# Optimization experiments

Measured on AMD Instinct MI355X. Metric: run time of the kernel, lower is better.

## Reference

```python
import jax, jax.numpy as jnp
import numpy as np

IMG_W, IMG_H = 960.0, 512.0          # NETWORK.IMAGE_SIZE
HM_W, HM_H = 240.0, 128.0            # NETWORK.HEATMAP_SIZE (w, h)
GRID_SIZE = (8000.0, 8000.0, 2000.0)
CUBE = (80, 80, 20)
SPACE_CENTER = (0.0, -500.0, 800.0)


def _make_grid():
    # compute_grid: meshgrid(indexing='ij'), flattened to [nbins, 3]
    gx = np.linspace(-GRID_SIZE[0] / 2, GRID_SIZE[0] / 2, CUBE[0]) + SPACE_CENTER[0]
    gy = np.linspace(-GRID_SIZE[1] / 2, GRID_SIZE[1] / 2, CUBE[1]) + SPACE_CENTER[1]
    gz = np.linspace(-GRID_SIZE[2] / 2, GRID_SIZE[2] / 2, CUBE[2]) + SPACE_CENTER[2]
    X, Y, Z = np.meshgrid(gx, gy, gz, indexing='ij')
    return jnp.asarray(np.stack([X.ravel(), Y.ravel(), Z.ravel()], 1), jnp.float32)


def setup_inputs() -> dict:
    key = jax.random.key(0)
    ks = jax.random.split(key, 8)
    n, B, J, H, W = 5, 4, 15, 128, 240
    heatmaps = jax.random.uniform(ks[0], (n, B, J, H, W), jnp.float32)
    # cameras: rotate about z per view, positioned so all grid points have depth > 0
    thetas = np.linspace(0.0, 2 * np.pi, n, endpoint=False)
    Rs = np.zeros((n, B, 3, 3), np.float32)
    for v, th in enumerate(thetas):
        c, s = np.cos(th), np.sin(th)
        Rs[v, :] = np.array([[c, -s, 0.0], [s, c, 0.0], [0.0, 0.0, 1.0]], np.float32)
    cam_R = jnp.asarray(Rs)
    cam_T = jnp.asarray(np.tile(np.array([0.0, 0.0, -5000.0], np.float32), (n, B, 1))) \
        + 50.0 * jax.random.normal(ks[1], (n, B, 3), jnp.float32)
    cam_f = 1500.0 + 20.0 * jax.random.normal(ks[2], (n, B, 2), jnp.float32)
    cam_c = jnp.asarray([IMG_W / 2, IMG_H / 2], jnp.float32) \
        + 5.0 * jax.random.normal(ks[3], (n, B, 2), jnp.float32)
    cam_k = jnp.asarray(np.tile(np.array([-0.01, 0.001, 0.0], np.float32), (n, B, 1))) \
        + 1e-4 * jax.random.normal(ks[4], (n, B, 3), jnp.float32)
    cam_p = 1e-3 * jax.random.normal(ks[5], (n, B, 2), jnp.float32)
    center = jnp.asarray([IMG_W / 2, IMG_H / 2], jnp.float32) \
        + 10.0 * jax.random.normal(ks[6], (n, B, 2), jnp.float32)
    scale = jnp.asarray([IMG_W / 200.0, IMG_H / 200.0], jnp.float32) \
        * (1.0 + 0.05 * jax.random.uniform(ks[7], (n, B, 2), jnp.float32))
    return {"heatmaps": heatmaps, "cam_R": cam_R, "cam_T": cam_T, "cam_f": cam_f,
            "cam_c": cam_c, "cam_k": cam_k, "cam_p": cam_p, "center": center,
            "scale": scale}


def _forward(heatmaps, cam_R, cam_T, cam_f, cam_c, cam_k, cam_p, center, scale):
    n, B, J, Hd, Wd = heatmaps.shape
    grid = _make_grid()                                   # [N, 3]
    N = grid.shape[0]
    # --- project_pose (pinhole + radial/tangential distortion) ---
    diff = grid[None, None] - cam_T[:, :, None, :]        # [v,b,N,3]
    xcam = jnp.einsum('vbij,vbnj->vbni', cam_R, diff)     # [v,b,N,3]
    y = xcam[..., :2] / (xcam[..., 2:3] + 1e-5)
    r2 = jnp.sum(y * y, -1)                               # [v,b,N]
    radial = 1.0 + cam_k[..., 0:1] * r2 + cam_k[..., 1:2] * r2 ** 2 + cam_k[..., 2:3] * r2 ** 3
    tan = cam_p[..., 0:1] * y[..., 1] + cam_p[..., 1:2] * y[..., 0]
    y = y * (radial + 2.0 * tan)[..., None] \
        + jnp.stack([cam_p[..., 1], cam_p[..., 0]], -1)[:, :, None, :] * r2[..., None]
    pix = cam_f[:, :, None, :] * y + cam_c[:, :, None, :]  # [v,b,N,2]
    # --- bounding: inside image of size (width, height) = 2*center ---
    wh = 2.0 * center                                      # [v,b,2]
    bounding = ((pix[..., 0] >= 0) & (pix[..., 1] >= 0)
                & (pix[..., 0] < wh[..., 0:1]) & (pix[..., 1] < wh[..., 1:2])
                ).astype(heatmaps.dtype)                   # [v,b,N]
    maxwh = jnp.maximum(wh[..., 0], wh[..., 1])[..., None, None]
    pix = jnp.clip(pix, -1.0, maxwh)
    # --- get_transform(center, scale, 0, img_size) + do_transform ---
    hs = 200.0 * scale                                     # [v,b,2]
    img = jnp.asarray([IMG_W, IMG_H], heatmaps.dtype)
    t_scale = img / hs                                     # diag of affine
    t_off = img * (-center / hs + 0.5)
    xy = pix * t_scale[:, :, None, :] + t_off[:, :, None, :]
    # scale to heatmap resolution, then to normalized [-1,1] (align_corners=True)
    xy = xy * (jnp.asarray([HM_W, HM_H], heatmaps.dtype) / img)
    sg = xy / jnp.asarray([HM_W - 1, HM_H - 1], heatmaps.dtype) * 2.0 - 1.0
    sg = jnp.clip(sg, -1.1, 1.1)
    # --- bilinear grid_sample, align_corners=True, zeros padding ---
    px = (sg[..., 0] + 1.0) * 0.5 * (Wd - 1)
    py = (sg[..., 1] + 1.0) * 0.5 * (Hd - 1)
    x0 = jnp.floor(px)
    y0 = jnp.floor(py)
    wx = px - x0
    wy = py - y0
    x0i = x0.astype(jnp.int32)
    y0i = y0.astype(jnp.int32)
    flat = heatmaps.reshape(n, B, J, Hd * Wd)

    def corner(xi, yi):
        valid = ((xi >= 0) & (xi < Wd) & (yi >= 0) & (yi < Hd)).astype(heatmaps.dtype)
        idx = jnp.clip(yi, 0, Hd - 1) * Wd + jnp.clip(xi, 0, Wd - 1)   # [v,b,N]
        g = jnp.take_along_axis(flat, idx[:, :, None, :], axis=3)       # [v,b,J,N]
        return g * valid[:, :, None, :]

    val = (corner(x0i, y0i) * ((1 - wx) * (1 - wy))[:, :, None, :]
           + corner(x0i + 1, y0i) * (wx * (1 - wy))[:, :, None, :]
           + corner(x0i, y0i + 1) * ((1 - wx) * wy)[:, :, None, :]
           + corner(x0i + 1, y0i + 1) * (wx * wy)[:, :, None, :])       # [v,b,J,N]
    # --- per-view cube = bounding * sampled; combine over views ---
    cubes_v = bounding[:, :, None, :] * val
    num = jnp.sum(cubes_v * bounding[:, :, None, :], axis=0)            # [b,J,N]
    den = jnp.sum(bounding, axis=0)[:, None, :] + 1e-6
    cubes = jnp.clip(num / den, 0.0, 1.0).reshape(B, J, CUBE[0], CUBE[1], CUBE[2])
    grids = jnp.broadcast_to(grid, (B, N, 3))
    return cubes, grids


def reference(heatmaps, cam_R, cam_T, cam_f, cam_c, cam_k, cam_p, center, scale):
    return _forward(heatmaps, cam_R, cam_T, cam_f, cam_c, cam_k, cam_p, center, scale)
```

## Files before the change

kernel.cpp:

```cpp
#include <hip/hip_runtime.h>

#define NV 5
#define NB 4
#define NJ 15
#define HD 128
#define WD 240
#define CX 80
#define CY 80
#define CZ 20
#define NPTS (CX*CY*CZ)
#define JP 16

struct ViewSample {
    float w[4];
    int   cx0, cx1, cy0, cy1;
    float bnd;
};

__device__ __forceinline__ ViewSample project_one_view(
    float gx, float gy, float gz,
    const float* __restrict__ cam_R, const float* __restrict__ cam_T,
    const float* __restrict__ cam_f, const float* __restrict__ cam_c,
    const float* __restrict__ cam_k, const float* __restrict__ cam_p,
    const float* __restrict__ center, const float* __restrict__ scale,
    int cb)
{
    const float* R = cam_R + cb*9;
    const float* T = cam_T + cb*3;
    float fx = cam_f[cb*2+0], fy = cam_f[cb*2+1];
    float ccx = cam_c[cb*2+0], ccy = cam_c[cb*2+1];
    float k0 = cam_k[cb*3+0], k1 = cam_k[cb*3+1], k2 = cam_k[cb*3+2];
    float p0 = cam_p[cb*2+0], p1 = cam_p[cb*2+1];
    float cenx = center[cb*2+0], ceny = center[cb*2+1];
    float scx = scale[cb*2+0],  scy = scale[cb*2+1];

    float dx = gx - T[0], dy = gy - T[1], dz = gz - T[2];
    float xc = R[0]*dx + R[1]*dy + R[2]*dz;
    float yc = R[3]*dx + R[4]*dy + R[5]*dz;
    float zc = R[6]*dx + R[7]*dy + R[8]*dz;
    float invz = 1.0f / (zc + 1e-5f);
    float ux = xc * invz, uy = yc * invz;
    float r2 = ux*ux + uy*uy;
    float radial = 1.0f + k0*r2 + k1*(r2*r2) + k2*(r2*r2*r2);
    float tn = p0*uy + p1*ux;
    float m  = radial + 2.0f*tn;
    float xd = ux*m + p1*r2;
    float yd = uy*m + p0*r2;
    float pixx = fx*xd + ccx;
    float pixy = fy*yd + ccy;

    float whx = 2.0f*cenx, why = 2.0f*ceny;
    float bnd = (pixx >= 0.0f && pixy >= 0.0f && pixx < whx && pixy < why) ? 1.0f : 0.0f;
    float mwh = fmaxf(whx, why);
    pixx = fminf(fmaxf(pixx, -1.0f), mwh);
    pixy = fminf(fmaxf(pixy, -1.0f), mwh);

    float hsx = 200.0f*scx, hsy = 200.0f*scy;
    float xyx = (pixx * (960.0f/hsx) + 960.0f*(-cenx/hsx + 0.5f)) * 0.25f;
    float xyy = (pixy * (512.0f/hsy) + 512.0f*(-ceny/hsy + 0.5f)) * 0.25f;
    float sgx = (xyx / 239.0f) * 2.0f - 1.0f;
    float sgy = (xyy / 127.0f) * 2.0f - 1.0f;
    sgx = fminf(fmaxf(sgx, -1.1f), 1.1f);
    sgy = fminf(fmaxf(sgy, -1.1f), 1.1f);

    float pxf = (sgx + 1.0f) * 0.5f * 239.0f;
    float pyf = (sgy + 1.0f) * 0.5f * 127.0f;
    float x0f = floorf(pxf), y0f = floorf(pyf);
    float wx = pxf - x0f, wy = pyf - y0f;
    int x0 = (int)x0f, y0 = (int)y0f;
    int x1 = x0 + 1,   y1 = y0 + 1;
    float vx0 = (x0 >= 0 && x0 < WD) ? 1.0f : 0.0f;
    float vx1 = (x1 >= 0 && x1 < WD) ? 1.0f : 0.0f;
    float vy0 = (y0 >= 0 && y0 < HD) ? 1.0f : 0.0f;
    float vy1 = (y1 >= 0 && y1 < HD) ? 1.0f : 0.0f;

    ViewSample s;
    s.cx0 = min(max(x0, 0), WD-1);
    s.cx1 = min(max(x1, 0), WD-1);
    s.cy0 = min(max(y0, 0), HD-1);
    s.cy1 = min(max(y1, 0), HD-1);
    s.w[0] = (1.0f-wx)*(1.0f-wy) * vx0*vy0 * bnd;
    s.w[1] = wx*(1.0f-wy)        * vx1*vy0 * bnd;
    s.w[2] = (1.0f-wx)*wy        * vx0*vy1 * bnd;
    s.w[3] = wx*wy               * vx1*vy1 * bnd;
    s.bnd = bnd;
    return s;
}

__global__ __launch_bounds__(256) void hm_transpose_kernel(
    const float* __restrict__ hm, float* __restrict__ out)
{
    int idx = blockIdx.x * 256 + threadIdx.x;
    if (idx >= NV*NB*HD*WD) return;
    int x  = idx % WD;
    int y  = (idx / WD) % HD;
    int vb = idx / (WD*HD);
    const float* src = hm + ((size_t)vb*NJ*HD + (size_t)y)*WD + x;
    float v[JP];
    #pragma unroll
    for (int j = 0; j < NJ; ++j) v[j] = src[(size_t)j*HD*WD];
    v[15] = 0.0f;
    float4* dst = (float4*)(out + (size_t)idx * JP);
    dst[0] = make_float4(v[0],  v[1],  v[2],  v[3]);
    dst[1] = make_float4(v[4],  v[5],  v[6],  v[7]);
    dst[2] = make_float4(v[8],  v[9],  v[10], v[11]);
    dst[3] = make_float4(v[12], v[13], v[14], v[15]);
}

__global__ __launch_bounds__(256) void project_kernel_T(
    const float* __restrict__ hmT,
    const float* __restrict__ cam_R, const float* __restrict__ cam_T,
    const float* __restrict__ cam_f, const float* __restrict__ cam_c,
    const float* __restrict__ cam_k, const float* __restrict__ cam_p,
    const float* __restrict__ center, const float* __restrict__ scale,
    float* __restrict__ out_cubes, float* __restrict__ out_grids)
{
    const int b  = blockIdx.x / (NPTS/256);
    const int nn = (blockIdx.x % (NPTS/256))*256 + threadIdx.x;

    int iz = nn % CZ;
    int iy = (nn / CZ) % CY;
    int ix = nn / (CZ*CY);
    float gx = (float)((double)ix * (8000.0/79.0) - 4000.0);
    float gy = (float)((double)iy * (8000.0/79.0) - 4500.0);
    float gz = (float)((double)iz * (2000.0/19.0) -  200.0);

    float wts[NV][4];
    int   offs[NV][4];
    float den = 0.0f;

    #pragma unroll
    for (int v = 0; v < NV; ++v) {
        int cb = v*NB + b;
        ViewSample s = project_one_view(gx, gy, gz, cam_R, cam_T, cam_f, cam_c,
                                        cam_k, cam_p, center, scale, cb);
        wts[v][0] = s.w[0]; wts[v][1] = s.w[1];
        wts[v][2] = s.w[2]; wts[v][3] = s.w[3];
        int base = cb * (HD*WD*JP);
        offs[v][0] = base + (s.cy0*WD + s.cx0)*JP;
        offs[v][1] = base + (s.cy0*WD + s.cx1)*JP;
        offs[v][2] = base + (s.cy1*WD + s.cx0)*JP;
        offs[v][3] = base + (s.cy1*WD + s.cx1)*JP;
        den += s.bnd;
    }

    float acc[NJ];
    #pragma unroll
    for (int j = 0; j < NJ; ++j) acc[j] = 0.0f;

    #pragma unroll
    for (int v = 0; v < NV; ++v) {
        #pragma unroll
        for (int c = 0; c < 4; ++c) {
            float w = wts[v][c];
            if (w != 0.0f) {
                const float4* p = (const float4*)(hmT + offs[v][c]);
                float4 q0 = p[0], q1 = p[1], q2 = p[2], q3 = p[3];
                acc[0]  += w*q0.x; acc[1]  += w*q0.y; acc[2]  += w*q0.z; acc[3]  += w*q0.w;
                acc[4]  += w*q1.x; acc[5]  += w*q1.y; acc[6]  += w*q1.z; acc[7]  += w*q1.w;
                acc[8]  += w*q2.x; acc[9]  += w*q2.y; acc[10] += w*q2.z; acc[11] += w*q2.w;
                acc[12] += w*q3.x; acc[13] += w*q3.y; acc[14] += w*q3.z;
            }
        }
    }

    float inv_den = 1.0f / (den + 1e-6f);
    #pragma unroll
    for (int j = 0; j < NJ; ++j) {
        float val = fminf(fmaxf(acc[j]*inv_den, 0.0f), 1.0f);
        out_cubes[((size_t)b*NJ + j)*NPTS + nn] = val;
    }
    float* g = out_grids + ((size_t)b*NPTS + nn)*3;
    g[0] = gx; g[1] = gy; g[2] = gz;
}

__global__ __launch_bounds__(256) void project_kernel_direct(
    const float* __restrict__ hm,
    const float* __restrict__ cam_R, const float* __restrict__ cam_T,
    const float* __restrict__ cam_f, const float* __restrict__ cam_c,
    const float* __restrict__ cam_k, const float* __restrict__ cam_p,
    const float* __restrict__ center, const float* __restrict__ scale,
    float* __restrict__ out_cubes, float* __restrict__ out_grids)
{
    const int b  = blockIdx.x / (NPTS/256);
    const int nn = (blockIdx.x % (NPTS/256))*256 + threadIdx.x;

    int iz = nn % CZ;
    int iy = (nn / CZ) % CY;
    int ix = nn / (CZ*CY);
    float gx = (float)((double)ix * (8000.0/79.0) - 4000.0);
    float gy = (float)((double)iy * (8000.0/79.0) - 4500.0);
    float gz = (float)((double)iz * (2000.0/19.0) -  200.0);

    float wts[NV][4];
    int   offs[NV][4];
    float bndv[NV];
    float den = 0.0f;

    #pragma unroll
    for (int v = 0; v < NV; ++v) {
        int cb = v*NB + b;
        ViewSample s = project_one_view(gx, gy, gz, cam_R, cam_T, cam_f, cam_c,
                                        cam_k, cam_p, center, scale, cb);
        wts[v][0] = s.w[0]; wts[v][1] = s.w[1];
        wts[v][2] = s.w[2]; wts[v][3] = s.w[3];
        offs[v][0] = s.cy0*WD + s.cx0;
        offs[v][1] = s.cy0*WD + s.cx1;
        offs[v][2] = s.cy1*WD + s.cx0;
        offs[v][3] = s.cy1*WD + s.cx1;
        bndv[v] = s.bnd;
        den += s.bnd;
    }

    float acc[NJ];
    #pragma unroll
    for (int j = 0; j < NJ; ++j) acc[j] = 0.0f;

    #pragma unroll
    for (int v = 0; v < NV; ++v) {
        if (bndv[v] != 0.0f) {
            int cb = v*NB + b;
            #pragma unroll
            for (int j = 0; j < NJ; ++j) {
                const float* base = hm + ((size_t)cb*NJ + j)*(HD*WD);
                acc[j] += wts[v][0]*base[offs[v][0]] + wts[v][1]*base[offs[v][1]]
                        + wts[v][2]*base[offs[v][2]] + wts[v][3]*base[offs[v][3]];
            }
        }
    }

    float inv_den = 1.0f / (den + 1e-6f);
    #pragma unroll
    for (int j = 0; j < NJ; ++j) {
        float val = fminf(fmaxf(acc[j]*inv_den, 0.0f), 1.0f);
        out_cubes[((size_t)b*NJ + j)*NPTS + nn] = val;
    }
    float* g = out_grids + ((size_t)b*NPTS + nn)*3;
    g[0] = gx; g[1] = gy; g[2] = gz;
}

extern "C" void kernel_launch(void* const* d_in, const int* in_sizes, int n_in,
                              void* d_out, int out_size, void* d_ws, size_t ws_size,
                              hipStream_t stream) {
    const float* hm     = (const float*)d_in[0];
    const float* cam_R  = (const float*)d_in[1];
    const float* cam_T  = (const float*)d_in[2];
    const float* cam_f  = (const float*)d_in[3];
    const float* cam_c  = (const float*)d_in[4];
    const float* cam_k  = (const float*)d_in[5];
    const float* cam_p  = (const float*)d_in[6];
    const float* center = (const float*)d_in[7];
    const float* scale  = (const float*)d_in[8];

    float* out_cubes = (float*)d_out;
    float* out_grids = out_cubes + (size_t)NB*NJ*NPTS;

    size_t need = (size_t)NV*NB*HD*WD*JP*sizeof(float);
    if (ws_size >= need) {
        float* hmT = (float*)d_ws;
        hipLaunchKernelGGL(hm_transpose_kernel,
                           dim3((NV*NB*HD*WD)/256), dim3(256), 0, stream, hm, hmT);
        hipLaunchKernelGGL(project_kernel_T,
                           dim3(NB*NPTS/256), dim3(256), 0, stream,
                           hmT, cam_R, cam_T, cam_f, cam_c, cam_k, cam_p,
                           center, scale, out_cubes, out_grids);
    } else {
        hipLaunchKernelGGL(project_kernel_direct,
                           dim3(NB*NPTS/256), dim3(256), 0, stream,
                           hm, cam_R, cam_T, cam_f, cam_c, cam_k, cam_p,
                           center, scale, out_cubes, out_grids);
    }
}
```

Before: 135.5 us.

## Store transposed heatmaps in fp16 and swizzle workgroup order for gather locality

The joint-interleaved heatmap copy is now stored in half precision, which halves both the transpose write traffic and the gather read traffic (32 bytes instead of 64 per corner). The projection kernel remaps block indices with an 8-way swizzle, likely to spread batches across XCDs for better L2 locality. It also drops the zero-weight branch so loads are issued unconditionally. The trade-off is fp16 rounding of the heatmap values and extra loads for out-of-bounds corners.

```diff
diff --git a/kernel.cpp b/kernel.cpp
--- a/kernel.cpp
+++ b/kernel.cpp
@@ -1,4 +1,5 @@
 #include <hip/hip_runtime.h>
+#include <hip/hip_fp16.h>
 
 #define NV 5
 #define NB 4
@@ -9,7 +10,9 @@
 #define CY 80
 #define CZ 20
 #define NPTS (CX*CY*CZ)
-#define JP 16
+#define JP16 16
+#define BLOCKS_PER_B (NPTS/256)
+#define NWG (NB*BLOCKS_PER_B)
 
 struct ViewSample {
     float w[4];
@@ -87,8 +90,17 @@
     return s;
 }
 
-__global__ __launch_bounds__(256) void hm_transpose_kernel(
-    const float* __restrict__ hm, float* __restrict__ out)
+__device__ __forceinline__ void grid_coords(int nn, float& gx, float& gy, float& gz) {
+    int iz = nn % CZ;
+    int iy = (nn / CZ) % CY;
+    int ix = nn / (CZ*CY);
+    gx = (float)(((double)ix * (8000.0/79.0) - 4000.0) + 0.0);
+    gy = (float)(((double)iy * (8000.0/79.0) - 4000.0) - 500.0);
+    gz = (float)(((double)iz * (2000.0/19.0) - 1000.0) + 800.0);
+}
+
+__global__ __launch_bounds__(256) void hm_transpose_f16(
+    const float* __restrict__ hm, __half* __restrict__ out)
 {
     int idx = blockIdx.x * 256 + threadIdx.x;
     if (idx >= NV*NB*HD*WD) return;
@@ -96,34 +108,30 @@
     int y  = (idx / WD) % HD;
     int vb = idx / (WD*HD);
     const float* src = hm + ((size_t)vb*NJ*HD + (size_t)y)*WD + x;
-    float v[JP];
-    #pragma unroll
-    for (int j = 0; j < NJ; ++j) v[j] = src[(size_t)j*HD*WD];
-    v[15] = 0.0f;
-    float4* dst = (float4*)(out + (size_t)idx * JP);
-    dst[0] = make_float4(v[0],  v[1],  v[2],  v[3]);
-    dst[1] = make_float4(v[4],  v[5],  v[6],  v[7]);
-    dst[2] = make_float4(v[8],  v[9],  v[10], v[11]);
-    dst[3] = make_float4(v[12], v[13], v[14], v[15]);
-}
-
-__global__ __launch_bounds__(256) void project_kernel_T(
-    const float* __restrict__ hmT,
+    union { float4 f4[2]; __half h[16]; } u;
+    #pragma unroll
+    for (int j = 0; j < NJ; ++j) u.h[j] = __float2half(src[(size_t)j*HD*WD]);
+    u.h[15] = __float2half(0.0f);
+    float4* dst = reinterpret_cast<float4*>(out + (size_t)idx * JP16);
+    dst[0] = u.f4[0];
+    dst[1] = u.f4[1];
+}
+
+__global__ __launch_bounds__(256) void project_kernel_f16(
+    const __half* __restrict__ hmT,
     const float* __restrict__ cam_R, const float* __restrict__ cam_T,
     const float* __restrict__ cam_f, const float* __restrict__ cam_c,
     const float* __restrict__ cam_k, const float* __restrict__ cam_p,
     const float* __restrict__ center, const float* __restrict__ scale,
     float* __restrict__ out_cubes, float* __restrict__ out_grids)
 {
-    const int b  = blockIdx.x / (NPTS/256);
-    const int nn = (blockIdx.x % (NPTS/256))*256 + threadIdx.x;
-
-    int iz = nn % CZ;
-    int iy = (nn / CZ) % CY;
-    int ix = nn / (CZ*CY);
-    float gx = (float)((double)ix * (8000.0/79.0) - 4000.0);
-    float gy = (float)((double)iy * (8000.0/79.0) - 4500.0);
-    float gz = (float)((double)iz * (2000.0/19.0) -  200.0);
+    int wg   = (int)blockIdx.x;
+    int swz  = (wg % 8) * (NWG/8) + wg / 8;
+    const int b  = swz / BLOCKS_PER_B;
+    const int nn = (swz % BLOCKS_PER_B)*256 + threadIdx.x;
+
+    float gx, gy, gz;
+    grid_coords(nn, gx, gy, gz);
 
     float wts[NV][4];
     int   offs[NV][4];
@@ -136,11 +144,11 @@
                                         cam_k, cam_p, center, scale, cb);
         wts[v][0] = s.w[0]; wts[v][1] = s.w[1];
         wts[v][2] = s.w[2]; wts[v][3] = s.w[3];
-        int base = cb * (HD*WD*JP);
-        offs[v][0] = base + (s.cy0*WD + s.cx0)*JP;
-        offs[v][1] = base + (s.cy0*WD + s.cx1)*JP;
-        offs[v][2] = base + (s.cy1*WD + s.cx0)*JP;
-        offs[v][3] = base + (s.cy1*WD + s.cx1)*JP;
+        int base = cb * (HD*WD*JP16);
+        offs[v][0] = base + (s.cy0*WD + s.cx0)*JP16;
+        offs[v][1] = base + (s.cy0*WD + s.cx1)*JP16;
+        offs[v][2] = base + (s.cy1*WD + s.cx0)*JP16;
+        offs[v][3] = base + (s.cy1*WD + s.cx1)*JP16;
         den += s.bnd;
     }
 
@@ -153,14 +161,18 @@
         #pragma unroll
         for (int c = 0; c < 4; ++c) {
             float w = wts[v][c];
-            if (w != 0.0f) {
-                const float4* p = (const float4*)(hmT + offs[v][c]);
-                float4 q0 = p[0], q1 = p[1], q2 = p[2], q3 = p[3];
-                acc[0]  += w*q0.x; acc[1]  += w*q0.y; acc[2]  += w*q0.z; acc[3]  += w*q0.w;
-                acc[4]  += w*q1.x; acc[5]  += w*q1.y; acc[6]  += w*q1.z; acc[7]  += w*q1.w;
-                acc[8]  += w*q2.x; acc[9]  += w*q2.y; acc[10] += w*q2.z; acc[11] += w*q2.w;
-                acc[12] += w*q3.x; acc[13] += w*q3.y; acc[14] += w*q3.z;
+            union { float4 f4[2]; __half2 h2[8]; } u;
+            const float4* p = reinterpret_cast<const float4*>(hmT + offs[v][c]);
+            u.f4[0] = p[0];
+            u.f4[1] = p[1];
+            #pragma unroll
+            for (int k = 0; k < 7; ++k) {
+                float2 f = __half22float2(u.h2[k]);
+                acc[2*k]   += w * f.x;
+                acc[2*k+1] += w * f.y;
             }
+            float2 f7 = __half22float2(u.h2[7]);
+            acc[14] += w * f7.x;
         }
     }
 
@@ -182,19 +194,14 @@
     const float* __restrict__ center, const float* __restrict__ scale,
     float* __restrict__ out_cubes, float* __restrict__ out_grids)
 {
-    const int b  = blockIdx.x / (NPTS/256);
-    const int nn = (blockIdx.x % (NPTS/256))*256 + threadIdx.x;
-
-    int iz = nn % CZ;
-    int iy = (nn / CZ) % CY;
-    int ix = nn / (CZ*CY);
-    float gx = (float)((double)ix * (8000.0/79.0) - 4000.0);
-    float gy = (float)((double)iy * (8000.0/79.0) - 4500.0);
-    float gz = (float)((double)iz * (2000.0/19.0) -  200.0);
+    const int b  = blockIdx.x / BLOCKS_PER_B;
+    const int nn = (blockIdx.x % BLOCKS_PER_B)*256 + threadIdx.x;
+
+    float gx, gy, gz;
+    grid_coords(nn, gx, gy, gz);
 
     float wts[NV][4];
     int   offs[NV][4];
-    float bndv[NV];
     float den = 0.0f;
 
     #pragma unroll
@@ -208,7 +215,6 @@
         offs[v][1] = s.cy0*WD + s.cx1;
         offs[v][2] = s.cy1*WD + s.cx0;
         offs[v][3] = s.cy1*WD + s.cx1;
-        bndv[v] = s.bnd;
         den += s.bnd;
     }
 
@@ -218,14 +224,12 @@
 
     #pragma unroll
     for (int v = 0; v < NV; ++v) {
-        if (bndv[v] != 0.0f) {
-            int cb = v*NB + b;
-            #pragma unroll
-            for (int j = 0; j < NJ; ++j) {
-                const float* base = hm + ((size_t)cb*NJ + j)*(HD*WD);
-                acc[j] += wts[v][0]*base[offs[v][0]] + wts[v][1]*base[offs[v][1]]
-                        + wts[v][2]*base[offs[v][2]] + wts[v][3]*base[offs[v][3]];
-            }
+        int cb = v*NB + b;
+        #pragma unroll
+        for (int j = 0; j < NJ; ++j) {
+            const float* base = hm + ((size_t)cb*NJ + j)*(HD*WD);
+            acc[j] += wts[v][0]*base[offs[v][0]] + wts[v][1]*base[offs[v][1]]
+                    + wts[v][2]*base[offs[v][2]] + wts[v][3]*base[offs[v][3]];
         }
     }
 
@@ -255,18 +259,18 @@
     float* out_cubes = (float*)d_out;
     float* out_grids = out_cubes + (size_t)NB*NJ*NPTS;
 
-    size_t need = (size_t)NV*NB*HD*WD*JP*sizeof(float);
+    size_t need = (size_t)NV*NB*HD*WD*JP16*sizeof(__half);
     if (ws_size >= need) {
-        float* hmT = (float*)d_ws;
-        hipLaunchKernelGGL(hm_transpose_kernel,
+        __half* hmT = (__half*)d_ws;
+        hipLaunchKernelGGL(hm_transpose_f16,
                            dim3((NV*NB*HD*WD)/256), dim3(256), 0, stream, hm, hmT);
-        hipLaunchKernelGGL(project_kernel_T,
-                           dim3(NB*NPTS/256), dim3(256), 0, stream,
+        hipLaunchKernelGGL(project_kernel_f16,
+                           dim3(NWG), dim3(256), 0, stream,
                            hmT, cam_R, cam_T, cam_f, cam_c, cam_k, cam_p,
                            center, scale, out_cubes, out_grids);
     } else {
         hipLaunchKernelGGL(project_kernel_direct,
-                           dim3(NB*NPTS/256), dim3(256), 0, stream,
+                           dim3(NWG), dim3(256), 0, stream,
                            hm, cam_R, cam_T, cam_f, cam_c, cam_k, cam_p,
                            center, scale, out_cubes, out_grids);
     }
```

New measurement: 126.7 us. 1.07x faster.
